# Kernel optimization log

Hardware: AMD Instinct MI355X
Metric: run time of the kernel (lower is better)

Reference implementation:

```python
import jax, jax.numpy as jnp
import numpy as np
from jax import lax

N, C, H, W = 32, 256, 56, 56
SHIFT = 2  # p_5_1_0, frozen random.randint(-3,3)

def setup_inputs() -> dict:
    key = jax.random.key(0)
    k1, k2, k3 = jax.random.split(key, 3)
    x = jax.random.normal(k1, (N, C, H, W), dtype=jnp.float32)
    w6 = jax.random.normal(k2, (C, 1), dtype=jnp.float32) * 0.1  # trunc_normal(std=0.1) approx
    w7 = jax.random.normal(k3, (C, C * 25), dtype=jnp.float32) * (1.0 / np.sqrt(C * 25))
    return {"x": x, "w6": w6, "w7": w7}

def reference(x, w6, w7):
    # t_1: max over width -> (n,c,h)
    t1 = jnp.max(x, axis=3)
    # t_3/t_4: relu then tanh
    t4 = jnp.tanh(jax.nn.relu(x))
    # t_5: roll along height axis
    t5 = jnp.roll(x, SHIFT, axis=2)
    # t_6: einsum 'abcd,be->aecd' with e=1 -> (n,h,w)
    t6 = jnp.einsum('nchw,c->nhw', t4, w6[:, 0])
    # t_2 + p_7: unfold(5x5, dilation=3, padding=6) + 1x1 conv == dilated 5x5 conv.
    # unfold channel ordering is c*25 + (kh*5+kw), so reshape to OIHW directly.
    conv_w = w7.reshape(C, C, 5, 5)
    t7 = lax.conv_general_dilated(
        x, conv_w, window_strides=(1, 1), padding=[(6, 6), (6, 6)],
        rhs_dilation=(3, 3), dimension_numbers=('NCHW', 'OIHW', 'NCHW'))
    t8 = x * t7
    # t_9: softmax over width of (n,h,w)
    t9 = jax.nn.softmax(t6, axis=2)
    t10 = t9[:, None, :, :] * t5
    t11 = t10 + t8
    return t1[:, :, :, None] - t11
```

## Files before the change

### kernel.cpp

```cpp
#include <hip/hip_runtime.h>
#include <hip/hip_bf16.h>
#include <math.h>

typedef __bf16 bf16x8 __attribute__((ext_vector_type(8)));
typedef short  s16x8  __attribute__((ext_vector_type(8)));
typedef float  f32x4  __attribute__((ext_vector_type(4)));
typedef unsigned short u16;

#define NN 32
#define CC 256
#define HH 56
#define WW 56
#define HP 68
#define XP2_BYTES 75759616ull
#define XP2_OFF 0ull
#define WT3_OFF 75759616ull
#define T1_OFF  79036416ull
#define T9_OFF  80871424ull

__device__ inline u16 f2bf(float f) {
    unsigned int u = __builtin_bit_cast(unsigned int, f);
    u = (u + 0x7fffu + ((u >> 16) & 1u)) >> 16;
    return (u16)u;
}

__device__ inline void gl_lds16(const char* g, char* l) {
    __builtin_amdgcn_global_load_lds(
        (const __attribute__((address_space(1))) unsigned int*)g,
        (__attribute__((address_space(3))) unsigned int*)l, 16, 0, 0);
}

__global__ void zero_halo(u16* __restrict__ xp2) {
    const int total = NN * 1488 * 32;
    int i = blockIdx.x * blockDim.x + threadIdx.x;
    const int stride = gridDim.x * blockDim.x;
    uint4 z; z.x = z.y = z.z = z.w = 0u;
    for (; i < total; i += stride) {
        int chunk = i & 31;
        int pid = i >> 5;
        int n = pid / 1488;
        int hp = pid - n * 1488;
        int row, col;
        if (hp < 816) { int r = hp / 68; col = hp - r * 68; row = (r < 6) ? r : r + 56; }
        else { int hq = hp - 816; int rr = hq / 12; int c12 = hq - rr * 12;
               row = 6 + rr; col = (c12 < 6) ? c12 : c12 + 56; }
        *(uint4*)((char*)xp2 + ((((size_t)n * HP + row) * HP + col) * 512) + chunk * 16) = z;
    }
}

__global__ __launch_bounds__(256)
void pack_w(const float* __restrict__ w7, u16* __restrict__ wt3) {
    int idx = blockIdx.x * 256 + threadIdx.x;
    int c_out = idx / 6400;
    int k = idx - c_out * 6400;
    int cin = k / 25;
    int tap = k - cin * 25;
    int kn = tap * 8 + (cin >> 5);
    int ci = cin & 31;
    int wr = c_out >> 7, mi = (c_out >> 4) & 7, mrow = c_out & 15;
    int ph = mi >> 2, mis = mi & 3;
    int q = ci >> 3, j = ci & 7;
    wt3[(size_t)kn * 8192 + ph * 4096 + wr * 2048 + mis * 512
        + (q * 16 + mrow) * 8 + j] = f2bf(w7[idx]);
}

__global__ __launch_bounds__(256)
void t169p(const float* __restrict__ x, const float* __restrict__ w6,
           float* __restrict__ t1, float* __restrict__ t9,
           u16* __restrict__ xp2) {
    const int n = blockIdx.x / HH;
    const int h = blockIdx.x % HH;
    const int wave = threadIdx.x >> 6;
    const int lane = threadIdx.x & 63;
    const bool valid = lane < WW;
    const int wl = valid ? lane : (WW - 1);
    const float* xrow = x + ((size_t)(n * CC) * HH + h) * WW;
    float a0 = 0.f, a1 = 0.f, a2 = 0.f, a3 = 0.f;
    __shared__ float sbuf[4 * 64];
    for (int i0 = 0; i0 < 64; i0 += 4) {
        const int c = wave * 64 + i0;
        float x0 = xrow[(size_t)(c + 0) * (HH * WW) + wl];
        float x1 = xrow[(size_t)(c + 1) * (HH * WW) + wl];
        float x2 = xrow[(size_t)(c + 2) * (HH * WW) + wl];
        float x3 = xrow[(size_t)(c + 3) * (HH * WW) + wl];
        float m0 = valid ? x0 : -INFINITY;
        float m1 = valid ? x1 : -INFINITY;
        float m2 = valid ? x2 : -INFINITY;
        float m3 = valid ? x3 : -INFINITY;
#pragma unroll
        for (int off = 32; off > 0; off >>= 1) {
            m0 = fmaxf(m0, __shfl_xor(m0, off));
            m1 = fmaxf(m1, __shfl_xor(m1, off));
            m2 = fmaxf(m2, __shfl_xor(m2, off));
            m3 = fmaxf(m3, __shfl_xor(m3, off));
        }
        if (lane == 0) {
            t1[(size_t)(n * CC + c + 0) * HH + h] = m0;
            t1[(size_t)(n * CC + c + 1) * HH + h] = m1;
            t1[(size_t)(n * CC + c + 2) * HH + h] = m2;
            t1[(size_t)(n * CC + c + 3) * HH + h] = m3;
        }
        if (valid) {
            a0 += tanhf(fmaxf(x0, 0.f)) * w6[c + 0];
            a1 += tanhf(fmaxf(x1, 0.f)) * w6[c + 1];
            a2 += tanhf(fmaxf(x2, 0.f)) * w6[c + 2];
            a3 += tanhf(fmaxf(x3, 0.f)) * w6[c + 3];
        }
    }
    sbuf[wave * 64 + lane] = (a0 + a1) + (a2 + a3);
    __syncthreads();
    if (wave == 0) {
        float s = sbuf[lane] + sbuf[64 + lane] + sbuf[128 + lane] + sbuf[192 + lane];
        float sm = valid ? s : -INFINITY;
        float mx = sm;
#pragma unroll
        for (int off = 32; off > 0; off >>= 1)
            mx = fmaxf(mx, __shfl_xor(mx, off));
        float e = valid ? expf(s - mx) : 0.f;
        float tot = e;
#pragma unroll
        for (int off = 32; off > 0; off >>= 1)
            tot += __shfl_xor(tot, off);
        if (valid) t9[((size_t)n * HH + h) * WW + lane] = e / tot;
    }
    u16* dst = xp2 + (((size_t)n * HP + h + 6) * HP + 6) * CC;
    for (int id = threadIdx.x; id < WW * 32; id += 256) {
        int p = id >> 5, oct = id & 31;
        s16x8 pk;
#pragma unroll
        for (int j = 0; j < 8; ++j)
            pk[j] = (short)f2bf(xrow[(size_t)(oct * 8 + j) * (HH * WW) + p]);
        *(s16x8*)(dst + (size_t)p * CC + oct * 8) = pk;
    }
}

__global__ __launch_bounds__(512, 2)
void conv_main(const char* __restrict__ xp2b, const char* __restrict__ wt3b,
               const float* __restrict__ x, const float* __restrict__ t1,
               const float* __restrict__ t9, float* __restrict__ out) {
    extern __shared__ __align__(16) char smem[];
    const int bid = blockIdx.x;
    const int tile = (bid & 7) * 49 + (bid >> 3);
    const int tid  = threadIdx.x;
    const int wid  = tid >> 6;
    const int lane = tid & 63;
    const int m = lane & 15;
    const int q = lane >> 4;
    const int wr = wid >> 2;
    const int wc = wid & 3;

    unsigned vb[2];
#pragma unroll
    for (int i = 0; i < 2; ++i) {
        int u = wid * 2 + i;
        int p = tile * 256 + (u >> 2) * 64 + (u & 3) * 16 + m;
        int n = p / (HH * WW);
        int rem = p - n * (HH * WW);
        int hh = rem / WW;
        int ww = rem - hh * WW;
        vb[i] = ((((unsigned)n * HP + hh + 6) * HP) + ww + 6) * 512 + q * 16;
    }
    const unsigned aoffS = wid * 1024 + lane * 16;

    auto stageA = [&](int tt, int ph) {
        const int kn = (tt < 200) ? tt : (tt - 200);
        char* d = smem + (size_t)(tt & 3) * 32768 + ph * 8192 + aoffS;
        const char* g = wt3b + (size_t)kn * 16384 + ph * 8192 + aoffS;
        gl_lds16(g, d);
    };
    auto stageB = [&](int tt, int i) {
        const int kn = (tt < 200) ? tt : (tt - 200);
        const int tp = kn >> 3, ch = kn & 7;
        const char* gb = xp2b +
            (ptrdiff_t)((tp / 5) * 3 - 6) * (HP * 512) +
            (ptrdiff_t)((tp % 5) * 3 - 6) * 512 + ch * 64 + vb[i];
        char* d = smem + (size_t)(tt & 3) * 32768 + 16384 + (wid * 2 + i) * 1024 + lane * 16;
        gl_lds16(gb, d);
    };

    f32x4 acc[8][4];
#pragma unroll
    for (int mi = 0; mi < 8; ++mi)
#pragma unroll
        for (int ni = 0; ni < 4; ++ni) {
            acc[mi][ni][0] = 0.f; acc[mi][ni][1] = 0.f;
            acc[mi][ni][2] = 0.f; acc[mi][ni][3] = 0.f;
        }

    const int aoff = wr * 4096 + lane * 16;
    const int boff = 16384 + wc * 4096 + lane * 16;

#pragma unroll
    for (int tt = 0; tt < 3; ++tt) {
        stageA(tt, 0); stageB(tt, 0);
        stageA(tt, 1); stageB(tt, 1);
    }
    asm volatile("s_waitcnt vmcnt(8)" ::: "memory");
    __builtin_amdgcn_s_barrier();

    for (int t = 0; t < 200; ++t) {
        const char* bp = smem + (size_t)(t & 3) * 32768;
        bf16x8 av[4], bv[4];

        stageA(t + 3, 0); stageB(t + 3, 0);
#pragma unroll
        for (int ni = 0; ni < 4; ++ni)
            bv[ni] = *(const bf16x8*)(const void*)(bp + boff + ni * 1024);
#pragma unroll
        for (int mi = 0; mi < 4; ++mi)
            av[mi] = *(const bf16x8*)(const void*)(bp + aoff + mi * 1024);
        __builtin_amdgcn_s_setprio(1);
#pragma unroll
        for (int mi = 0; mi < 4; ++mi)
#pragma unroll
            for (int ni = 0; ni < 4; ++ni)
                acc[mi][ni] = __builtin_amdgcn_mfma_f32_16x16x32_bf16(
                    av[mi], bv[ni], acc[mi][ni], 0, 0, 0);
        __builtin_amdgcn_s_setprio(0);

        stageA(t + 3, 1); stageB(t + 3, 1);
#pragma unroll
        for (int mi = 0; mi < 4; ++mi)
            av[mi] = *(const bf16x8*)(const void*)(bp + aoff + 8192 + mi * 1024);
        __builtin_amdgcn_s_setprio(1);
#pragma unroll
        for (int mi = 0; mi < 4; ++mi)
#pragma unroll
            for (int ni = 0; ni < 4; ++ni)
                acc[mi + 4][ni] = __builtin_amdgcn_mfma_f32_16x16x32_bf16(
                    av[mi], bv[ni], acc[mi + 4][ni], 0, 0, 0);
        __builtin_amdgcn_s_setprio(0);
        asm volatile("s_waitcnt vmcnt(8)" ::: "memory");
        __builtin_amdgcn_s_barrier();
    }

#pragma unroll
    for (int ni = 0; ni < 4; ++ni) {
        const int p = tile * 256 + wc * 64 + ni * 16 + m;
        const int n = p / (HH * WW);
        const int rem = p - n * (HH * WW);
        const int h = rem / WW;
        const int w = rem - h * WW;
        const float t9v = t9[((size_t)n * HH + h) * WW + w];
        const int hprev = (h >= 2) ? (h - 2) : (h + HH - 2);
#pragma unroll
        for (int mi = 0; mi < 8; ++mi) {
            const int c = wr * 128 + mi * 16 + q * 4;
#pragma unroll
            for (int r = 0; r < 4; ++r) {
                const size_t rowi = (size_t)(n * CC + c + r) * HH;
                const float t1v = t1[rowi + h];
                const float xv = x[(rowi + h) * WW + w];
                const float xr = x[(rowi + hprev) * WW + w];
                out[(rowi + h) * WW + w] = t1v - (t9v * xr + xv * acc[mi][ni][r]);
            }
        }
    }
}

extern "C" void kernel_launch(void* const* d_in, const int* in_sizes, int n_in,
                              void* d_out, int out_size, void* d_ws, size_t ws_size,
                              hipStream_t stream) {
    const float* x  = (const float*)d_in[0];
    const float* w6 = (const float*)d_in[1];
    const float* w7 = (const float*)d_in[2];
    float* out = (float*)d_out;
    char* ws = (char*)d_ws;
    u16*   xp2 = (u16*)(ws + XP2_OFF);
    u16*   wt3 = (u16*)(ws + WT3_OFF);
    float* t1  = (float*)(ws + T1_OFF);
    float* t9  = (float*)(ws + T9_OFF);

    static bool lds_cfg_done = false;
    if (!lds_cfg_done) {
        (void)hipFuncSetAttribute((const void*)conv_main,
                                  hipFuncAttributeMaxDynamicSharedMemorySize,
                                  131072);
        lds_cfg_done = true;
    }

    zero_halo<<<dim3(1024), dim3(256), 0, stream>>>(xp2);
    pack_w<<<dim3(6400), dim3(256), 0, stream>>>(w7, wt3);
    t169p<<<dim3(NN * HH), dim3(256), 0, stream>>>(x, w6, t1, t9, xp2);
    conv_main<<<dim3(392), dim3(512), 131072, stream>>>((const char*)xp2, (const char*)wt3,
                                                        x, t1, t9, out);
}
```

Baseline: 627.2 us.

## Switch conv GEMM to 32x32x16 MFMA and split x packing into LDS-transposed kernel

The main convolution GEMM moves from 16x16x32 MFMA tiles to 32x32x16 MFMA tiles. Weight packing and the B-operand staging layouts are rewritten to match, and the epilogue row mapping changes accordingly. The larger tile should cut LDS reads per FLOP. Packing x to padded bf16 NHWC moves into its own kernel that transposes through shared memory for coalesced reads. tanh is replaced by an exp/rcp formula, which gives up a little accuracy for cheaper math.

```diff
diff --git a/kernel.cpp b/kernel.cpp
--- a/kernel.cpp
+++ b/kernel.cpp
@@ -4,7 +4,7 @@
 
 typedef __bf16 bf16x8 __attribute__((ext_vector_type(8)));
 typedef short  s16x8  __attribute__((ext_vector_type(8)));
-typedef float  f32x4  __attribute__((ext_vector_type(4)));
+typedef float  f32x16 __attribute__((ext_vector_type(16)));
 typedef unsigned short u16;
 
 #define NN 32
@@ -56,18 +56,16 @@
     int cin = k / 25;
     int tap = k - cin * 25;
     int kn = tap * 8 + (cin >> 5);
-    int ci = cin & 31;
-    int wr = c_out >> 7, mi = (c_out >> 4) & 7, mrow = c_out & 15;
-    int ph = mi >> 2, mis = mi & 3;
-    int q = ci >> 3, j = ci & 7;
-    wt3[(size_t)kn * 8192 + ph * 4096 + wr * 2048 + mis * 512
-        + (q * 16 + mrow) * 8 + j] = f2bf(w7[idx]);
+    int c5 = cin & 31;
+    int ks = c5 >> 4, half = (c5 >> 3) & 1, j = c5 & 7;
+    int lane = half * 32 + (c_out & 31);
+    int rb = c_out >> 5;
+    wt3[(size_t)kn * 8192 + ks * 4096 + rb * 512 + lane * 8 + j] = f2bf(w7[idx]);
 }
 
 __global__ __launch_bounds__(256)
-void t169p(const float* __restrict__ x, const float* __restrict__ w6,
-           float* __restrict__ t1, float* __restrict__ t9,
-           u16* __restrict__ xp2) {
+void t169(const float* __restrict__ x, const float* __restrict__ w6,
+          float* __restrict__ t1, float* __restrict__ t9) {
     const int n = blockIdx.x / HH;
     const int h = blockIdx.x % HH;
     const int wave = threadIdx.x >> 6;
@@ -101,10 +99,14 @@
             t1[(size_t)(n * CC + c + 3) * HH + h] = m3;
         }
         if (valid) {
-            a0 += tanhf(fmaxf(x0, 0.f)) * w6[c + 0];
-            a1 += tanhf(fmaxf(x1, 0.f)) * w6[c + 1];
-            a2 += tanhf(fmaxf(x2, 0.f)) * w6[c + 2];
-            a3 += tanhf(fmaxf(x3, 0.f)) * w6[c + 3];
+            float e0 = __expf(2.f * fmaxf(x0, 0.f));
+            float e1 = __expf(2.f * fmaxf(x1, 0.f));
+            float e2 = __expf(2.f * fmaxf(x2, 0.f));
+            float e3 = __expf(2.f * fmaxf(x3, 0.f));
+            a0 += (1.f - 2.f * __builtin_amdgcn_rcpf(e0 + 1.f)) * w6[c + 0];
+            a1 += (1.f - 2.f * __builtin_amdgcn_rcpf(e1 + 1.f)) * w6[c + 1];
+            a2 += (1.f - 2.f * __builtin_amdgcn_rcpf(e2 + 1.f)) * w6[c + 2];
+            a3 += (1.f - 2.f * __builtin_amdgcn_rcpf(e3 + 1.f)) * w6[c + 3];
         }
     }
     sbuf[wave * 64 + lane] = (a0 + a1) + (a2 + a3);
@@ -123,14 +125,36 @@
             tot += __shfl_xor(tot, off);
         if (valid) t9[((size_t)n * HH + h) * WW + lane] = e / tot;
     }
+}
+
+__global__ __launch_bounds__(256)
+void pack_x(const float* __restrict__ x, u16* __restrict__ xp2) {
+    const int n = blockIdx.x / HH;
+    const int h = blockIdx.x % HH;
+    const int lane = threadIdx.x & 63;
+    const int wid = threadIdx.x >> 6;
+    __shared__ u16 xbuf[64 * 66];
+    const float* xrow = x + ((size_t)(n * CC) * HH + h) * WW;
     u16* dst = xp2 + (((size_t)n * HP + h + 6) * HP + 6) * CC;
-    for (int id = threadIdx.x; id < WW * 32; id += 256) {
-        int p = id >> 5, oct = id & 31;
-        s16x8 pk;
-#pragma unroll
-        for (int j = 0; j < 8; ++j)
-            pk[j] = (short)f2bf(xrow[(size_t)(oct * 8 + j) * (HH * WW) + p]);
-        *(s16x8*)(dst + (size_t)p * CC + oct * 8) = pk;
+    for (int g = 0; g < 4; ++g) {
+        if (g) __syncthreads();
+        if (lane < WW) {
+            const int c0 = g * 64 + wid * 16;
+#pragma unroll
+            for (int r = 0; r < 16; ++r) {
+                float v = xrow[(size_t)(c0 + r) * (HH * WW) + lane];
+                xbuf[(wid * 16 + r) * 66 + lane] = f2bf(v);
+            }
+        }
+        __syncthreads();
+        for (int id = threadIdx.x; id < WW * 8; id += 256) {
+            int p = id >> 3, ch8 = id & 7;
+            s16x8 pk;
+#pragma unroll
+            for (int j = 0; j < 8; ++j)
+                pk[j] = (short)xbuf[(ch8 * 8 + j) * 66 + p];
+            *(s16x8*)(dst + (size_t)p * CC + g * 64 + ch8 * 8) = pk;
+        }
     }
 }
 
@@ -144,51 +168,50 @@
     const int tid  = threadIdx.x;
     const int wid  = tid >> 6;
     const int lane = tid & 63;
-    const int m = lane & 15;
-    const int q = lane >> 4;
+    const int l31 = lane & 31;
+    const int lhi = lane >> 5;
     const int wr = wid >> 2;
     const int wc = wid & 3;
 
-    unsigned vb[2];
-#pragma unroll
-    for (int i = 0; i < 2; ++i) {
-        int u = wid * 2 + i;
-        int p = tile * 256 + (u >> 2) * 64 + (u & 3) * 16 + m;
+    unsigned vb;
+    {
+        int p = tile * 256 + wid * 32 + l31;
         int n = p / (HH * WW);
         int rem = p - n * (HH * WW);
         int hh = rem / WW;
         int ww = rem - hh * WW;
-        vb[i] = ((((unsigned)n * HP + hh + 6) * HP) + ww + 6) * 512 + q * 16;
-    }
-    const unsigned aoffS = wid * 1024 + lane * 16;
-
-    auto stageA = [&](int tt, int ph) {
+        vb = ((((unsigned)n * HP + hh + 6) * HP) + ww + 6) * 512 + lhi * 16;
+    }
+
+    auto stageA = [&](int tt, int ks) {
         const int kn = (tt < 200) ? tt : (tt - 200);
-        char* d = smem + (size_t)(tt & 3) * 32768 + ph * 8192 + aoffS;
-        const char* g = wt3b + (size_t)kn * 16384 + ph * 8192 + aoffS;
+        const unsigned o = ks * 8192 + wid * 1024 + lane * 16;
+        char* d = smem + (size_t)(tt & 3) * 32768 + o;
+        const char* g = wt3b + (size_t)kn * 16384 + o;
         gl_lds16(g, d);
     };
-    auto stageB = [&](int tt, int i) {
+    auto stageB = [&](int tt, int ks) {
         const int kn = (tt < 200) ? tt : (tt - 200);
         const int tp = kn >> 3, ch = kn & 7;
         const char* gb = xp2b +
             (ptrdiff_t)((tp / 5) * 3 - 6) * (HP * 512) +
-            (ptrdiff_t)((tp % 5) * 3 - 6) * 512 + ch * 64 + vb[i];
-        char* d = smem + (size_t)(tt & 3) * 32768 + 16384 + (wid * 2 + i) * 1024 + lane * 16;
+            (ptrdiff_t)((tp % 5) * 3 - 6) * 512 + ch * 64 + ks * 32 + vb;
+        char* d = smem + (size_t)(tt & 3) * 32768 + 16384
+                  + ks * 8192 + wid * 1024 + lane * 16;
         gl_lds16(gb, d);
     };
 
-    f32x4 acc[8][4];
-#pragma unroll
-    for (int mi = 0; mi < 8; ++mi)
-#pragma unroll
-        for (int ni = 0; ni < 4; ++ni) {
-            acc[mi][ni][0] = 0.f; acc[mi][ni][1] = 0.f;
-            acc[mi][ni][2] = 0.f; acc[mi][ni][3] = 0.f;
-        }
+    f32x16 acc[4][2];
+#pragma unroll
+    for (int mi = 0; mi < 4; ++mi)
+#pragma unroll
+        for (int nb = 0; nb < 2; ++nb)
+#pragma unroll
+            for (int r = 0; r < 16; ++r)
+                acc[mi][nb][r] = 0.f;
 
     const int aoff = wr * 4096 + lane * 16;
-    const int boff = 16384 + wc * 4096 + lane * 16;
+    const int boff = 16384 + wc * 2048 + lane * 16;
 
 #pragma unroll
     for (int tt = 0; tt < 3; ++tt) {
@@ -200,43 +223,33 @@
 
     for (int t = 0; t < 200; ++t) {
         const char* bp = smem + (size_t)(t & 3) * 32768;
-        bf16x8 av[4], bv[4];
-
-        stageA(t + 3, 0); stageB(t + 3, 0);
-#pragma unroll
-        for (int ni = 0; ni < 4; ++ni)
-            bv[ni] = *(const bf16x8*)(const void*)(bp + boff + ni * 1024);
-#pragma unroll
-        for (int mi = 0; mi < 4; ++mi)
-            av[mi] = *(const bf16x8*)(const void*)(bp + aoff + mi * 1024);
-        __builtin_amdgcn_s_setprio(1);
-#pragma unroll
-        for (int mi = 0; mi < 4; ++mi)
-#pragma unroll
-            for (int ni = 0; ni < 4; ++ni)
-                acc[mi][ni] = __builtin_amdgcn_mfma_f32_16x16x32_bf16(
-                    av[mi], bv[ni], acc[mi][ni], 0, 0, 0);
-        __builtin_amdgcn_s_setprio(0);
-
-        stageA(t + 3, 1); stageB(t + 3, 1);
-#pragma unroll
-        for (int mi = 0; mi < 4; ++mi)
-            av[mi] = *(const bf16x8*)(const void*)(bp + aoff + 8192 + mi * 1024);
-        __builtin_amdgcn_s_setprio(1);
-#pragma unroll
-        for (int mi = 0; mi < 4; ++mi)
-#pragma unroll
-            for (int ni = 0; ni < 4; ++ni)
-                acc[mi + 4][ni] = __builtin_amdgcn_mfma_f32_16x16x32_bf16(
-                    av[mi], bv[ni], acc[mi + 4][ni], 0, 0, 0);
-        __builtin_amdgcn_s_setprio(0);
+        bf16x8 av[4], bv[2];
+
+#pragma unroll
+        for (int ks = 0; ks < 2; ++ks) {
+            stageA(t + 3, ks); stageB(t + 3, ks);
+#pragma unroll
+            for (int nb = 0; nb < 2; ++nb)
+                bv[nb] = *(const bf16x8*)(const void*)(bp + boff + ks * 8192 + nb * 1024);
+#pragma unroll
+            for (int mi = 0; mi < 4; ++mi)
+                av[mi] = *(const bf16x8*)(const void*)(bp + aoff + ks * 8192 + mi * 1024);
+            __builtin_amdgcn_s_setprio(1);
+#pragma unroll
+            for (int mi = 0; mi < 4; ++mi)
+#pragma unroll
+                for (int nb = 0; nb < 2; ++nb)
+                    acc[mi][nb] = __builtin_amdgcn_mfma_f32_32x32x16_bf16(
+                        av[mi], bv[nb], acc[mi][nb], 0, 0, 0);
+            __builtin_amdgcn_s_setprio(0);
+        }
         asm volatile("s_waitcnt vmcnt(8)" ::: "memory");
         __builtin_amdgcn_s_barrier();
     }
 
 #pragma unroll
-    for (int ni = 0; ni < 4; ++ni) {
-        const int p = tile * 256 + wc * 64 + ni * 16 + m;
+    for (int nb = 0; nb < 2; ++nb) {
+        const int p = tile * 256 + wc * 64 + nb * 32 + l31;
         const int n = p / (HH * WW);
         const int rem = p - n * (HH * WW);
         const int h = rem / WW;
@@ -244,15 +257,16 @@
         const float t9v = t9[((size_t)n * HH + h) * WW + w];
         const int hprev = (h >= 2) ? (h - 2) : (h + HH - 2);
 #pragma unroll
-        for (int mi = 0; mi < 8; ++mi) {
-            const int c = wr * 128 + mi * 16 + q * 4;
-#pragma unroll
-            for (int r = 0; r < 4; ++r) {
-                const size_t rowi = (size_t)(n * CC + c + r) * HH;
+        for (int mi = 0; mi < 4; ++mi) {
+            const int c0 = wr * 128 + mi * 32 + 4 * lhi;
+#pragma unroll
+            for (int r = 0; r < 16; ++r) {
+                const int c = c0 + (r & 3) + 8 * (r >> 2);
+                const size_t rowi = (size_t)(n * CC + c) * HH;
                 const float t1v = t1[rowi + h];
                 const float xv = x[(rowi + h) * WW + w];
                 const float xr = x[(rowi + hprev) * WW + w];
-                out[(rowi + h) * WW + w] = t1v - (t9v * xr + xv * acc[mi][ni][r]);
+                out[(rowi + h) * WW + w] = t1v - (t9v * xr + xv * acc[mi][nb][r]);
             }
         }
     }
@@ -281,7 +295,8 @@
 
     zero_halo<<<dim3(1024), dim3(256), 0, stream>>>(xp2);
     pack_w<<<dim3(6400), dim3(256), 0, stream>>>(w7, wt3);
-    t169p<<<dim3(NN * HH), dim3(256), 0, stream>>>(x, w6, t1, t9, xp2);
+    t169<<<dim3(NN * HH), dim3(256), 0, stream>>>(x, w6, t1, t9);
+    pack_x<<<dim3(NN * HH), dim3(256), 0, stream>>>(x, xp2);
     conv_main<<<dim3(392), dim3(512), 131072, stream>>>((const char*)xp2, (const char*)wt3,
                                                         x, t1, t9, out);
 }
```

Measured after the change: 618.5 us. About the same (-1.4%).
